# Optimization experiments

Measured on AMD Instinct MI355X. Metric: run time of the kernel, lower is better.

Reference implementation:

```python
import jax, jax.numpy as jnp
import numpy as np

B, D, H, K = 16384, 128, 1024, 8
OPD = 3 * K + 1  # params per dim
TB = 3.0         # tail_bound: left=bottom=-TB, right=top=TB
EPS = 1e-12
MIN_W = MIN_H = MIN_D = 1e-3


def _masks():
    rng = np.random.RandomState(0)
    in_deg = np.arange(1, D + 1)
    h1 = rng.randint(1, D, size=(H,))
    h2 = rng.randint(1, D, size=(H,))
    out_deg = np.arange(1, D + 1)
    m1 = (in_deg[None, :] <= h1[:, None]).astype(np.float32)          # [H, D]
    m2 = (h1[None, :] <= h2[:, None]).astype(np.float32)              # [H, H]
    m3 = np.repeat((out_deg[:, None] > h2[None, :]).astype(np.float32), OPD, axis=0)  # [D*OPD, H]
    return jnp.asarray(m1), jnp.asarray(m2), jnp.asarray(m3)


def _kaiming(key, fan_out, fan_in, a=0.1):
    bound = np.sqrt(6.0 / ((1.0 + a * a) * fan_in))
    return jax.random.uniform(key, (fan_out, fan_in), jnp.float32, -bound, bound)


def setup_inputs() -> dict:
    key = jax.random.key(0)
    kx, k1, k2, k3 = jax.random.split(key, 4)
    m1, m2, m3 = _masks()
    return {
        'x': jax.random.normal(kx, (B, D), jnp.float32),
        'W1': _kaiming(k1, H, D), 'b1': jnp.zeros((H,), jnp.float32),
        'W2': _kaiming(k2, H, H), 'b2': jnp.zeros((H,), jnp.float32),
        'W3': _kaiming(k3, D * OPD, H), 'b3': jnp.zeros((D * OPD,), jnp.float32),
        'm1': m1, 'm2': m2, 'm3': m3,
    }


def _norm_cum(u, mn):
    k = u.shape[-1]
    w = jax.nn.softmax(u, axis=-1)
    w = mn + (1.0 - mn * k) * w
    c = jnp.cumsum(w, axis=-1)
    c = jnp.pad(c, [(0, 0)] * (c.ndim - 1) + [(1, 0)])
    c = c / jnp.clip(c[..., -1:], 1e-12)
    return c[..., 1:] - c[..., :-1], c


def _take(p, idx):
    return jnp.take_along_axis(p, idx[..., None], axis=-1)[..., 0]


def _forward(x, W1, b1, W2, b2, W3, b3, m1, m2, m3):
    h = jax.nn.silu(x @ (W1 * m1).T + b1)
    h = jax.nn.silu(h @ (W2 * m2).T + b2)
    raw = (h @ (W3 * m3).T + b3).reshape(-1, D, OPD)  # [B, D, 3K+1]
    uw, uh, ud = raw[..., :K], raw[..., K:2 * K], raw[..., 2 * K:]
    w, cw = _norm_cum(uw, MIN_W)
    hh, ch = _norm_cum(uh, MIN_H)
    d = MIN_D + jax.nn.softplus(ud)  # [B, D, K+1]

    left, right, bottom, top = -TB, TB, -TB, TB
    inside = (x >= left) & (x <= right)  # [B, D]
    xs = jnp.clip((x - left) / (right - left), 0.0, 1.0)
    bid = jnp.clip(jnp.sum((xs[..., None] >= cw), axis=-1) - 1, 0, K - 1)
    xk, wk = _take(cw, bid), _take(w, bid)
    yk, hk = _take(ch, bid), _take(hh, bid)
    dk, dk1 = _take(d, bid), _take(d, bid + 1)
    t = jnp.clip((xs - xk) / (wk + EPS), 0.0, 1.0)
    a = (hk + EPS) / (wk + EPS)
    num = a * t * t + dk * t * (1 - t)
    den = a + (dk + dk1 - 2 * a) * t * (1 - t)
    s = num / (den + EPS)
    y = (yk + hk * s) * (top - bottom) + bottom
    dnum = a * a * (dk1 * t * t + 2 * a * t * (1 - t) + dk * (1 - t) * (1 - t))
    dydx = (top - bottom) / (right - left) * dnum / (den * den + EPS)
    out = jnp.where(inside, y, x)
    lad = jnp.where(inside, jnp.log(jnp.clip(dydx, 1e-12)), 0.0)
    return out, jnp.sum(lad, axis=-1)


def reference(x, W1, b1, W2, b2, W3, b3, m1, m2, m3):
    return _forward(x, W1, b1, W2, b2, W3, b3, m1, m2, m3)
```

## Files before the change

kernel.cpp:

```cpp
#include <hip/hip_runtime.h>
#include <hip/hip_bf16.h>

#define BATCH 16384
#define DIM   128
#define HID   1024
#define NK    8
#define OPD   25
#define N3    (DIM*OPD)
#define NP    3328

typedef __attribute__((ext_vector_type(8))) short  short8;
typedef __attribute__((ext_vector_type(4))) float  floatx4;
typedef unsigned int u32;

__device__ __forceinline__ float fexp(float x) { return __expf(x); }
__device__ __forceinline__ float flog(float x) { return __logf(x); }
__device__ __forceinline__ float fdiv(float a, float b) { return __fdividef(a, b); }

__device__ __forceinline__ void async_copy16(const unsigned short* g,
                                             unsigned short* l) {
    __builtin_amdgcn_global_load_lds(
        (const __attribute__((address_space(1))) u32*)g,
        (__attribute__((address_space(3))) u32*)l,
        16, 0, 0);
}

__device__ __forceinline__ void stage_slot(const unsigned short* __restrict__ A,
                                           const unsigned short* __restrict__ Bw,
                                           unsigned short* As, unsigned short* Bs,
                                           size_t abase, size_t bbase,
                                           int Kd, int kc, int w, int lane) {
    const int rsub = lane >> 2;
    const int csw  = ((lane & 3) ^ ((lane >> 3) & 3)) * 8;
    #pragma unroll
    for (int p = 0; p < 2; p++) {
        const int q = w * 2 + p;
        async_copy16(&A[abase + (size_t)(q * 16 + rsub) * Kd + kc + csw],
                     &As[q * 512 + lane * 8]);
        async_copy16(&Bw[bbase + (size_t)(q * 16 + rsub) * Kd + kc + csw],
                     &Bs[q * 512 + lane * 8]);
    }
}

__device__ __forceinline__ void compute_slot(const unsigned short* As,
                                             const unsigned short* Bs,
                                             int wr, int wc, int lr, int quad,
                                             floatx4 acc[4][4]) {
    const int csel = (quad ^ ((lr >> 1) & 3)) * 8;
    short8 af[4], bfr[4];
    #pragma unroll
    for (int i = 0; i < 4; i++)
        af[i] = *(const short8*)&As[(wr + i * 16 + lr) * 32 + csel];
    #pragma unroll
    for (int j = 0; j < 4; j++)
        bfr[j] = *(const short8*)&Bs[(wc + j * 16 + lr) * 32 + csel];
    #pragma unroll
    for (int i = 0; i < 4; i++)
        #pragma unroll
        for (int j = 0; j < 4; j++)
            acc[i][j] = __builtin_amdgcn_mfma_f32_16x16x32_bf16(
                af[i], bfr[j], acc[i][j], 0, 0, 0);
}

#define KLOOP_DB(A_, B_, abase_, bbase_, Kd_, Klim_)                          \
    if (Klim_ > 0) {                                                          \
        stage_slot(A_, B_, As0, Bs0, abase_, bbase_, Kd_, 0, w, lane);        \
        for (int k0 = 0; k0 < Klim_; k0 += 64) {                              \
            asm volatile("s_waitcnt vmcnt(0) lgkmcnt(0)" ::: "memory");       \
            __builtin_amdgcn_s_barrier();                                     \
            stage_slot(A_, B_, As1, Bs1, abase_, bbase_, Kd_, k0 + 32, w, lane);\
            compute_slot(As0, Bs0, wr, wc, lr, quad, acc);                    \
            asm volatile("s_waitcnt vmcnt(0) lgkmcnt(0)" ::: "memory");       \
            __builtin_amdgcn_s_barrier();                                     \
            if (k0 + 64 < Klim_)                                              \
                stage_slot(A_, B_, As0, Bs0, abase_, bbase_, Kd_, k0 + 64, w, lane);\
            compute_slot(As1, Bs1, wr, wc, lr, quad, acc);                    \
        }                                                                     \
    }

__global__ __launch_bounds__(128) void hsum_kernel(
    const float* __restrict__ m1, const float* __restrict__ m3,
    int* __restrict__ h1i, int* __restrict__ h2i) {
    const int b = blockIdx.x, t = threadIdx.x;
    if (b < HID) {
        float v = m1[b * DIM + t];
        #pragma unroll
        for (int off = 32; off > 0; off >>= 1) v += __shfl_down(v, off, 64);
        __shared__ float ws[2];
        if ((t & 63) == 0) ws[t >> 6] = v;
        __syncthreads();
        if (t == 0) h1i[b] = (int)(ws[0] + ws[1] + 0.5f);
    } else {
        const int j = (b - HID) * 128 + t;
        float s = 0.f;
        for (int d = 0; d < DIM; d++) s += m3[(size_t)d * OPD * HID + j];
        h2i[j] = DIM - (int)(s + 0.5f);
    }
}

__global__ __launch_bounds__(1024) void sort_kernel(
    const int* __restrict__ h1i, const int* __restrict__ h2i,
    int* __restrict__ perm1, int* __restrict__ perm2,
    int* __restrict__ h1sv, int* __restrict__ h2sv,
    int* __restrict__ klim1, int* __restrict__ klim2, int* __restrict__ klim3)
{
    __shared__ int hist[128];
    __shared__ int h1s[1024], h2s[1024];
    const int t = threadIdx.x;
    const int h1v = h1i[t], h2v = h2i[t];

    if (t < 128) hist[t] = 0;
    __syncthreads();
    atomicAdd(&hist[h1v], 1);
    __syncthreads();
    if (t == 0) { int a = 0; for (int b = 0; b < 128; b++) { int c = hist[b]; hist[b] = a; a += c; } }
    __syncthreads();
    int r = atomicAdd(&hist[h1v], 1);
    perm1[r] = t; h1s[r] = h1v; h1sv[r] = h1v;
    __syncthreads();
    if (t < 128) hist[t] = 0;
    __syncthreads();
    atomicAdd(&hist[h2v], 1);
    __syncthreads();
    if (t == 0) { int a = 0; for (int b = 0; b < 128; b++) { int c = hist[b]; hist[b] = a; a += c; } }
    __syncthreads();
    r = atomicAdd(&hist[h2v], 1);
    perm2[r] = t; h2s[r] = h2v; h2sv[r] = h2v;
    __syncthreads();

    if (t < 8) {
        klim1[t] = ((h1s[t * 128 + 127] + 63) >> 6) << 6;
        int mh = h2s[t * 128 + 127];
        int c = 0;
        for (int j = 0; j < 1024; j++) c += (h1s[j] <= mh) ? 1 : 0;
        klim2[t] = ((c + 63) >> 6) << 6;
    }
    if (t < 26) {
        int dmax = t * 5 + 4; if (dmax > 127) dmax = 127;
        int c = 0;
        for (int j = 0; j < 1024; j++) c += (h2s[j] <= dmax) ? 1 : 0;
        klim3[t] = ((c + 63) >> 6) << 6;
    }
}

__global__ __launch_bounds__(256) void wperm_kernel(
    const float* __restrict__ W1, const float* __restrict__ b1,
    const float* __restrict__ W2, const float* __restrict__ b2,
    const float* __restrict__ W3, const float* __restrict__ x,
    const int* __restrict__ perm1, const int* __restrict__ perm2,
    const int* __restrict__ h1sv, const int* __restrict__ h2sv,
    __hip_bfloat16* __restrict__ w1p, float* __restrict__ b1p,
    __hip_bfloat16* __restrict__ w2p, float* __restrict__ b2p,
    __hip_bfloat16* __restrict__ w3p,
    __hip_bfloat16* __restrict__ xb, float* __restrict__ lad)
{
    __shared__ float row[HID];
    const int b = blockIdx.x, t = threadIdx.x;
    if (b < 512) {
        const int i = b * 256 + t;
        const int hp = i >> 7, col = i & 127;
        const int src = perm1[hp];
        float v = (col < h1sv[hp]) ? W1[src * DIM + col] : 0.f;
        w1p[i] = __float2bfloat16(v);
        if (col == 0) b1p[hp] = b1[src];
    } else if (b < 512 + HID) {
        const int ip = b - 512;
        const int si = perm2[ip];
        const int h2v = h2sv[ip];
        #pragma unroll
        for (int q = 0; q < 4; q++) row[q * 256 + t] = W2[(size_t)si * HID + q * 256 + t];
        __syncthreads();
        #pragma unroll
        for (int q = 0; q < 4; q++) {
            const int jp = q * 256 + t;
            float v = (h1sv[jp] <= h2v) ? row[perm1[jp]] : 0.f;
            w2p[(size_t)ip * HID + jp] = __float2bfloat16(v);
        }
        if (t == 0) b2p[ip] = b2[si];
    } else if (b < 512 + HID + NP) {
        const int c = b - 512 - HID;
        const int s = c & 127, t3 = c >> 7;
        if (s >= 125) {
            #pragma unroll
            for (int q = 0; q < 4; q++)
                w3p[(size_t)c * HID + q * 256 + t] = __float2bfloat16(0.f);
            return;
        }
        const int srcrow = t3 * 125 + s;
        const int d = srcrow / 25;
        #pragma unroll
        for (int q = 0; q < 4; q++) row[q * 256 + t] = W3[(size_t)srcrow * HID + q * 256 + t];
        __syncthreads();
        #pragma unroll
        for (int q = 0; q < 4; q++) {
            const int kk = q * 256 + t;
            float v = (h2sv[kk] <= d) ? row[perm2[kk]] : 0.f;
            w3p[(size_t)c * HID + kk] = __float2bfloat16(v);
        }
    } else {
        const int i = (b - (512 + HID + NP)) * 256 + t;
        xb[i] = __float2bfloat16(x[i]);
        if (i < BATCH) lad[i] = 0.f;
    }
}

__device__ __forceinline__ void spline_eval(const float* __restrict__ p,
                                            float xv, float& yout, float& lout) {
    float cw[NK + 1], ch[NK + 1];
    {
        float mx = p[0];
        #pragma unroll
        for (int j = 1; j < NK; j++) mx = fmaxf(mx, p[j]);
        float e[NK], s = 0.f;
        #pragma unroll
        for (int j = 0; j < NK; j++) { e[j] = fexp(p[j] - mx); s += e[j]; }
        const float inv = fdiv(1.f, s);
        cw[0] = 0.f;
        #pragma unroll
        for (int j = 0; j < NK; j++) cw[j + 1] = cw[j] + (0.001f + 0.992f * e[j] * inv);
    }
    {
        float mx = p[8];
        #pragma unroll
        for (int j = 1; j < NK; j++) mx = fmaxf(mx, p[8 + j]);
        float e[NK], s = 0.f;
        #pragma unroll
        for (int j = 0; j < NK; j++) { e[j] = fexp(p[8 + j] - mx); s += e[j]; }
        const float inv = fdiv(1.f, s);
        ch[0] = 0.f;
        #pragma unroll
        for (int j = 0; j < NK; j++) ch[j + 1] = ch[j] + (0.001f + 0.992f * e[j] * inv);
    }
    const float icw = fdiv(1.f, fmaxf(cw[NK], 1e-12f));
    const float ich = fdiv(1.f, fmaxf(ch[NK], 1e-12f));

    const bool inside = (xv >= -3.f) && (xv <= 3.f);
    float xs = (xv + 3.f) * (1.f / 6.f);
    xs = fminf(fmaxf(xs, 0.f), 1.f);
    const float xsc = xs * cw[NK];

    float xk = 0.f, wk = cw[1], yk = 0.f, hk = ch[1];
    float uda = p[16], udb = p[17];
    #pragma unroll
    for (int j = 1; j < NK; j++) {
        const bool c = (xsc >= cw[j]);
        xk  = c ? cw[j] : xk;
        wk  = c ? (cw[j + 1] - cw[j]) : wk;
        yk  = c ? ch[j] : yk;
        hk  = c ? (ch[j + 1] - ch[j]) : hk;
        uda = c ? p[16 + j] : uda;
        udb = c ? p[17 + j] : udb;
    }
    xk *= icw; wk *= icw;
    yk *= ich; hk *= ich;

    const float dk  = 0.001f + ((uda > 20.f) ? uda : flog(1.f + fexp(uda)));
    const float dk1 = 0.001f + ((udb > 20.f) ? udb : flog(1.f + fexp(udb)));

    float t = fdiv(xs - xk, wk + 1e-12f);
    t = fminf(fmaxf(t, 0.f), 1.f);
    const float a   = fdiv(hk + 1e-12f, wk + 1e-12f);
    const float omt = 1.f - t;
    const float tt1 = t * omt;
    const float num = a * t * t + dk * tt1;
    const float den = a + (dk + dk1 - 2.f * a) * tt1;
    const float s   = fdiv(num, den + 1e-12f);
    const float y   = (yk + hk * s) * 6.f - 3.f;
    const float dnum = a * a * (dk1 * t * t + 2.f * a * tt1 + dk * omt * omt);
    const float dydx = fdiv(dnum, den * den + 1e-12f);

    yout = inside ? y : xv;
    lout = inside ? flog(fmaxf(dydx, 1e-12f)) : 0.f;
}

__global__ __launch_bounds__(256, 4) void gemm_bt_kernel(
    const unsigned short* __restrict__ A,
    const unsigned short* __restrict__ Bw,
    const float* __restrict__ bias,
    const int* __restrict__ klim,
    __hip_bfloat16* __restrict__ Cout,
    int M, int N, int Kd)
{
    __shared__ __align__(16) unsigned short sm[16384];
    unsigned short* const As0 = sm;
    unsigned short* const As1 = sm + 4096;
    unsigned short* const Bs0 = sm + 8192;
    unsigned short* const Bs1 = sm + 12288;

    const int bid = blockIdx.y * gridDim.x + blockIdx.x;
    const int GY  = (gridDim.y >= 16) ? 16 : gridDim.y;
    const int per_group = gridDim.x * GY;
    const int g  = bid / per_group;
    const int rr = bid % per_group;
    const int bn = (gridDim.x - 1 - rr / GY) * 128;
    const int bm = (g * GY + (rr % GY)) * 128;
    const int Klim = klim[bn >> 7];

    const int t    = threadIdx.x;
    const int lane = t & 63;
    const int w    = t >> 6;
    const int wr   = (w >> 1) * 64;
    const int wc   = (w & 1) * 64;
    const int lr   = lane & 15;
    const int quad = lane >> 4;

    floatx4 acc[4][4] = {};
    const size_t abase = (size_t)bm * Kd;
    const size_t bbase = (size_t)bn * Kd;

    KLOOP_DB(A, Bw, abase, bbase, Kd, Klim)

    #pragma unroll
    for (int j = 0; j < 4; j++) {
        const int col = bn + wc + j * 16 + lr;
        const float bv = bias[col];
        #pragma unroll
        for (int i = 0; i < 4; i++) {
            const int rowb = bm + wr + i * 16 + quad * 4;
            #pragma unroll
            for (int r = 0; r < 4; r++) {
                float v = acc[i][j][r] + bv;
                v = v * fdiv(1.f, 1.f + fexp(-v));
                Cout[(size_t)(rowb + r) * N + col] = __float2bfloat16(v);
            }
        }
    }
}

__global__ __launch_bounds__(256, 4) void gemm3_spline_kernel(
    const unsigned short* __restrict__ A,
    const unsigned short* __restrict__ Bw,
    const float* __restrict__ b3,
    const int* __restrict__ klim,
    const float* __restrict__ x,
    float* __restrict__ out,
    float* __restrict__ lad,
    int M)
{
    constexpr int Kd  = HID;
    constexpr int LSE = 126;
    __shared__ __align__(16) char smem[64 * LSE * 4 + 128 * 4];
    unsigned short* const sm  = (unsigned short*)smem;
    unsigned short* const As0 = sm;
    unsigned short* const As1 = sm + 4096;
    unsigned short* const Bs0 = sm + 8192;
    unsigned short* const Bs1 = sm + 12288;
    float* eb     = (float*)smem;
    float* ladacc = (float*)(smem + 64 * LSE * 4);

    const int bid = blockIdx.y * gridDim.x + blockIdx.x;
    const int GY  = 16;
    const int per_group = gridDim.x * GY;
    const int g  = bid / per_group;
    const int rr = bid % per_group;
    const int tile = 25 - rr / GY;
    const int bn = tile * 128;
    const int bm = (g * GY + (rr % GY)) * 128;
    const int Klim = klim[tile];

    const int t    = threadIdx.x;
    const int lane = t & 63;
    const int w    = t >> 6;
    const int wr   = (w >> 1) * 64;
    const int wc   = (w & 1) * 64;
    const int lr   = lane & 15;
    const int quad = lane >> 4;

    floatx4 acc[4][4] = {};
    const size_t abase = (size_t)bm * Kd;
    const size_t bbase = (size_t)bn * Kd;

    KLOOP_DB(A, Bw, abase, bbase, Kd, Klim)

    #pragma unroll 1
    for (int h = 0; h < 2; h++) {
        __syncthreads();
        if (h == 0 && t < 128) ladacc[t] = 0.f;
        if ((w >> 1) == h) {
            #pragma unroll
            for (int j = 0; j < 4; j++) {
                const int s = wc + j * 16 + lr;
                if (s < 125) {
                    const int bidx = tile * 125 + s;
                    const float bv = b3[bidx < N3 ? bidx : 0];
                    #pragma unroll
                    for (int i = 0; i < 4; i++) {
                        const int lrw = i * 16 + quad * 4;
                        #pragma unroll
                        for (int r2 = 0; r2 < 4; r2++)
                            eb[(lrw + r2) * LSE + s] = acc[i][j][r2] + bv;
                    }
                }
            }
        }
        __syncthreads();
        #pragma unroll 1
        for (int q = t; q < 320; q += 256) {
            const int r  = q / 5;
            const int ds = q % 5;
            const int dim = tile * 5 + ds;
            if (dim < DIM) {
                const float* p = eb + r * LSE + ds * 25;
                const int grow = bm + h * 64 + r;
                const float xv = x[(size_t)grow * DIM + dim];
                float y, l;
                spline_eval(p, xv, y, l);
                out[(size_t)grow * DIM + dim] = y;
                atomicAdd(&ladacc[h * 64 + r], l);
            }
        }
    }
    __syncthreads();
    if (t < 128) atomicAdd(&lad[bm + t], ladacc[t]);
}

extern "C" void kernel_launch(void* const* d_in, const int* in_sizes, int n_in,
                              void* d_out, int out_size, void* d_ws, size_t ws_size,
                              hipStream_t stream) {
    const float* x  = (const float*)d_in[0];
    const float* W1 = (const float*)d_in[1];
    const float* b1 = (const float*)d_in[2];
    const float* W2 = (const float*)d_in[3];
    const float* b2 = (const float*)d_in[4];
    const float* W3 = (const float*)d_in[5];
    const float* b3 = (const float*)d_in[6];
    const float* m1 = (const float*)d_in[7];
    const float* m3 = (const float*)d_in[9];

    char* ws = (char*)d_ws;
    const size_t OFF_W1B = 0;
    const size_t OFF_W2B = OFF_W1B + (size_t)HID * DIM * 2;
    const size_t OFF_W3P = OFF_W2B + (size_t)HID * HID * 2;
    const size_t OFF_XB  = OFF_W3P + (size_t)NP * HID * 2;
    const size_t OFF_H1B = OFF_XB  + (size_t)BATCH * DIM * 2;
    const size_t OFF_H2B = OFF_H1B + (size_t)BATCH * HID * 2;
    const size_t OFF_SML = OFF_H2B + (size_t)BATCH * HID * 2;

    __hip_bfloat16* w1p = (__hip_bfloat16*)(ws + OFF_W1B);
    __hip_bfloat16* w2p = (__hip_bfloat16*)(ws + OFF_W2B);
    __hip_bfloat16* w3p = (__hip_bfloat16*)(ws + OFF_W3P);
    __hip_bfloat16* xb  = (__hip_bfloat16*)(ws + OFF_XB);
    __hip_bfloat16* h1b = (__hip_bfloat16*)(ws + OFF_H1B);
    __hip_bfloat16* h2b = (__hip_bfloat16*)(ws + OFF_H2B);

    float* b1p   = (float*)(ws + OFF_SML);
    float* b2p   = b1p + HID;
    int*   h1i   = (int*)(b2p + HID);
    int*   h2i   = h1i + HID;
    int*   perm1 = h2i + HID;
    int*   perm2 = perm1 + HID;
    int*   h1sv  = perm2 + HID;
    int*   h2sv  = h1sv + HID;
    int*   klim1 = h2sv + HID;
    int*   klim2 = klim1 + 8;
    int*   klim3 = klim2 + 8;

    float* out_p = (float*)d_out;
    float* lad_p = out_p + (size_t)BATCH * DIM;

    hsum_kernel<<<HID + 8, 128, 0, stream>>>(m1, m3, h1i, h2i);
    sort_kernel<<<1, 1024, 0, stream>>>(h1i, h2i, perm1, perm2, h1sv, h2sv,
                                        klim1, klim2, klim3);
    wperm_kernel<<<512 + HID + NP + (BATCH * DIM) / 256, 256, 0, stream>>>(
        W1, b1, W2, b2, W3, x, perm1, perm2, h1sv, h2sv,
        w1p, b1p, w2p, b2p, w3p, xb, lad_p);

    gemm_bt_kernel<<<dim3(HID / 128, BATCH / 128), 256, 0, stream>>>(
        (const unsigned short*)xb, (const unsigned short*)w1p, b1p, klim1, h1b,
        BATCH, HID, DIM);
    gemm_bt_kernel<<<dim3(HID / 128, BATCH / 128), 256, 0, stream>>>(
        (const unsigned short*)h1b, (const unsigned short*)w2p, b2p, klim2, h2b,
        BATCH, HID, HID);
    gemm3_spline_kernel<<<dim3(NP / 128, BATCH / 128), 256, 0, stream>>>(
        (const unsigned short*)h2b, (const unsigned short*)w3p, b3, klim3, x,
        out_p, lad_p, BATCH);
}
```

Baseline: 277.4 us.

## Deepen GEMM K-loop to triple-buffered LDS pipeline with partial vmcnt waits

Replaces the double-buffered K loop with a three-stage rotating LDS ring. Two K-slices are kept in flight, and the loop waits with vmcnt(4) instead of draining all loads, so global-to-LDS copies overlap more with MFMA compute. It also cuts the loop to one barrier per 32-wide slice. In exchange, LDS per block grows from 32KB to 48KB, which may lower occupancy under launch_bounds(256,4). The vmcnt(4) count assumes stage_slot issues exactly four loads per thread.

Result: slower. 299.9 us (+8.1%).

```diff
diff --git a/kernel.cpp b/kernel.cpp
--- a/kernel.cpp
+++ b/kernel.cpp
@@ -62,20 +62,26 @@
                 af[i], bfr[j], acc[i][j], 0, 0, 0);
 }
 
-#define KLOOP_DB(A_, B_, abase_, bbase_, Kd_, Klim_)                          \
-    if (Klim_ > 0) {                                                          \
-        stage_slot(A_, B_, As0, Bs0, abase_, bbase_, Kd_, 0, w, lane);        \
-        for (int k0 = 0; k0 < Klim_; k0 += 64) {                              \
-            asm volatile("s_waitcnt vmcnt(0) lgkmcnt(0)" ::: "memory");       \
-            __builtin_amdgcn_s_barrier();                                     \
-            stage_slot(A_, B_, As1, Bs1, abase_, bbase_, Kd_, k0 + 32, w, lane);\
-            compute_slot(As0, Bs0, wr, wc, lr, quad, acc);                    \
-            asm volatile("s_waitcnt vmcnt(0) lgkmcnt(0)" ::: "memory");       \
-            __builtin_amdgcn_s_barrier();                                     \
-            if (k0 + 64 < Klim_)                                              \
-                stage_slot(A_, B_, As0, Bs0, abase_, bbase_, Kd_, k0 + 64, w, lane);\
-            compute_slot(As1, Bs1, wr, wc, lr, quad, acc);                    \
-        }                                                                     \
+#define KLOOP_3DEEP(A_, B_, abase_, bbase_, Kd_, Klim_)                        \
+    if (Klim_ > 0) {                                                           \
+        unsigned short *pa0 = As0, *pa1 = As1, *pa2 = As2;                     \
+        unsigned short *pb0 = Bs0, *pb1 = Bs1, *pb2 = Bs2;                     \
+        const int n_ = (Klim_) >> 5;                                           \
+        stage_slot(A_, B_, pa0, pb0, abase_, bbase_, Kd_, 0, w, lane);         \
+        stage_slot(A_, B_, pa1, pb1, abase_, bbase_, Kd_, 32, w, lane);        \
+        for (int i_ = 0; i_ + 1 < n_; ++i_) {                                  \
+            asm volatile("s_waitcnt vmcnt(4) lgkmcnt(0)" ::: "memory");        \
+            __builtin_amdgcn_s_barrier();                                      \
+            if (i_ + 2 < n_)                                                   \
+                stage_slot(A_, B_, pa2, pb2, abase_, bbase_, Kd_,              \
+                           (i_ + 2) * 32, w, lane);                            \
+            compute_slot(pa0, pb0, wr, wc, lr, quad, acc);                     \
+            unsigned short* tp_ = pa0; pa0 = pa1; pa1 = pa2; pa2 = tp_;        \
+            tp_ = pb0; pb0 = pb1; pb1 = pb2; pb2 = tp_;                        \
+        }                                                                      \
+        asm volatile("s_waitcnt vmcnt(0) lgkmcnt(0)" ::: "memory");            \
+        __builtin_amdgcn_s_barrier();                                          \
+        compute_slot(pa0, pb0, wr, wc, lr, quad, acc);                         \
     }
 
 __global__ __launch_bounds__(128) void hsum_kernel(
@@ -281,11 +287,13 @@
     __hip_bfloat16* __restrict__ Cout,
     int M, int N, int Kd)
 {
-    __shared__ __align__(16) unsigned short sm[16384];
+    __shared__ __align__(16) unsigned short sm[24576];
     unsigned short* const As0 = sm;
     unsigned short* const As1 = sm + 4096;
-    unsigned short* const Bs0 = sm + 8192;
-    unsigned short* const Bs1 = sm + 12288;
+    unsigned short* const As2 = sm + 8192;
+    unsigned short* const Bs0 = sm + 12288;
+    unsigned short* const Bs1 = sm + 16384;
+    unsigned short* const Bs2 = sm + 20480;
 
     const int bid = blockIdx.y * gridDim.x + blockIdx.x;
     const int GY  = (gridDim.y >= 16) ? 16 : gridDim.y;
@@ -308,7 +316,7 @@
     const size_t abase = (size_t)bm * Kd;
     const size_t bbase = (size_t)bn * Kd;
 
-    KLOOP_DB(A, Bw, abase, bbase, Kd, Klim)
+    KLOOP_3DEEP(A, Bw, abase, bbase, Kd, Klim)
 
     #pragma unroll
     for (int j = 0; j < 4; j++) {
@@ -339,12 +347,14 @@
 {
     constexpr int Kd  = HID;
     constexpr int LSE = 126;
-    __shared__ __align__(16) char smem[64 * LSE * 4 + 128 * 4];
+    __shared__ __align__(16) char smem[49152];
     unsigned short* const sm  = (unsigned short*)smem;
     unsigned short* const As0 = sm;
     unsigned short* const As1 = sm + 4096;
-    unsigned short* const Bs0 = sm + 8192;
-    unsigned short* const Bs1 = sm + 12288;
+    unsigned short* const As2 = sm + 8192;
+    unsigned short* const Bs0 = sm + 12288;
+    unsigned short* const Bs1 = sm + 16384;
+    unsigned short* const Bs2 = sm + 20480;
     float* eb     = (float*)smem;
     float* ladacc = (float*)(smem + 64 * LSE * 4);
 
@@ -370,7 +380,7 @@
     const size_t abase = (size_t)bm * Kd;
     const size_t bbase = (size_t)bn * Kd;
 
-    KLOOP_DB(A, Bw, abase, bbase, Kd, Klim)
+    KLOOP_3DEEP(A, Bw, abase, bbase, Kd, Klim)
 
     #pragma unroll 1
     for (int h = 0; h < 2; h++) {
```
